# Optimization experiments

Measured on AMD Instinct MI355X. Metric: run time of the kernel, lower is better.

The kernel has to match this reference:

```python
import jax, jax.numpy as jnp
import numpy as np

B, H, W, C = 16, 224, 224, 3
NP = 14                      # n_patches per side
PH = PW = H // NP            # 16
PATCH = PH * PW * C          # 768
D_MODEL = 512
EXPAND = 2
D_INNER = D_MODEL * EXPAND   # 1024
D_STATE = 16
D_CONV = 4
DT_RANK = -(-D_MODEL // 16)  # ceil(512/16) = 32
N_LAYERS = 4
N_CLASSES = 1000


def posemb_sincos_2d(h, w, dim, temperature=10000.0):
    y, x = jnp.meshgrid(jnp.arange(h, dtype=jnp.float32), jnp.arange(w, dtype=jnp.float32), indexing='ij')
    omega = jnp.arange(dim // 4, dtype=jnp.float32) / (dim // 4 - 1)
    omega = 1.0 / (temperature ** omega)
    yy = y.reshape(-1, 1) * omega[None, :]
    xx = x.reshape(-1, 1) * omega[None, :]
    return jnp.concatenate([jnp.sin(xx), jnp.cos(xx), jnp.sin(yy), jnp.cos(yy)], axis=1)  # [h*w, dim]


def setup_inputs() -> dict:
    key = jax.random.key(0)
    ks = jax.random.split(key, 12)
    s = 0.02
    inp = {
        'x': jax.random.normal(ks[0], (B, H, W, C), jnp.float32),
        'patch_w': jax.random.normal(ks[1], (PATCH, D_MODEL), jnp.float32) * s,
        'patch_b': jnp.zeros((D_MODEL,), jnp.float32),
        'norm_w': jnp.ones((N_LAYERS, D_MODEL), jnp.float32),
        'in_proj_w': jax.random.normal(ks[2], (N_LAYERS, D_MODEL, 2 * D_INNER), jnp.float32) * s,
        'conv_w': jax.random.normal(ks[3], (N_LAYERS, D_INNER, D_CONV), jnp.float32) * 0.1,
        'x_proj_w': jax.random.normal(ks[4], (N_LAYERS, D_INNER, DT_RANK + 2 * D_STATE), jnp.float32) * s,
        'dt_proj_w': jax.random.normal(ks[5], (N_LAYERS, DT_RANK, D_INNER), jnp.float32) * s,
        'dt_proj_b': jax.random.normal(ks[6], (N_LAYERS, D_INNER), jnp.float32) * 0.1,
        'A_log': jnp.broadcast_to(jnp.log(jnp.arange(1, D_STATE + 1, dtype=jnp.float32)), (N_LAYERS, D_INNER, D_STATE)) + 0.0,
        'D': jnp.ones((N_LAYERS, D_INNER), jnp.float32),
        'out_proj_w': jax.random.normal(ks[7], (N_LAYERS, D_INNER, D_MODEL), jnp.float32) * s,
        'head_w': jax.random.normal(ks[8], (D_MODEL, N_CLASSES), jnp.float32) * s,
        'head_b': jnp.zeros((N_CLASSES,), jnp.float32),
    }
    return inp


def rms_norm(x, w, eps=1e-5):
    return x * jax.lax.rsqrt(jnp.mean(x * x, axis=-1, keepdims=True) + eps) * w


def selective_scan(u, delta, A, Bm, Cm, Dv):
    # u, delta: [b,l,d]; A: [d,n]; Bm, Cm: [b,l,n]; Dv: [d]
    dA = jnp.exp(jnp.einsum('bld,dn->bldn', delta, A))          # [b,l,d,n]
    dBu = jnp.einsum('bld,bln->bldn', delta * u, Bm)            # [b,l,d,n]
    b, l, d = u.shape
    n = A.shape[1]

    def step(s, inp):
        dA_t, dBu_t, C_t = inp
        s = dA_t * s + dBu_t                                    # [b,d,n]
        y = jnp.einsum('bdn,bn->bd', s, C_t)
        return s, y

    s0 = jnp.zeros((b, d, n), u.dtype)
    _, ys = jax.lax.scan(step, s0, (dA.transpose(1, 0, 2, 3), dBu.transpose(1, 0, 2, 3), Cm.transpose(1, 0, 2)))
    y = ys.transpose(1, 0, 2)                                   # [b,l,d]
    return y + u * Dv


def mamba_block(x, in_w, conv_w, xp_w, dt_w, dt_b, A_log, Dv, out_w):
    b, l, _ = x.shape
    xr = x @ in_w                                               # [b,l,2*d_inner]
    xi, res = jnp.split(xr, 2, axis=-1)
    # causal depthwise conv over sequence
    xc = jax.lax.conv_general_dilated(
        xi.transpose(0, 2, 1),                                  # [b,d_inner,l]
        conv_w[:, None, :],                                     # [d_inner,1,k]
        window_strides=(1,), padding=[(D_CONV - 1, 0)],
        feature_group_count=D_INNER,
        dimension_numbers=('NCH', 'OIH', 'NCH'))
    xi = jax.nn.silu(xc.transpose(0, 2, 1))                     # [b,l,d_inner]
    A = -jnp.exp(A_log)
    x_dbl = xi @ xp_w                                           # [b,l,dt_rank+2n]
    delta, Bm, Cm = jnp.split(x_dbl, [DT_RANK, DT_RANK + D_STATE], axis=-1)
    delta = jax.nn.softplus(delta @ dt_w + dt_b)                # [b,l,d_inner]
    y = selective_scan(xi, delta, A, Bm, Cm, Dv)
    y = y * jax.nn.silu(res)
    return y @ out_w


def reference(x, patch_w, patch_b, norm_w, in_proj_w, conv_w, x_proj_w, dt_proj_w, dt_proj_b, A_log, D, out_proj_w, head_w, head_b):
    b = x.shape[0]
    # patchify: b (h ph) (w pw) c -> b (h w) (ph pw c)
    p = x.reshape(b, NP, PH, NP, PW, C).transpose(0, 1, 3, 2, 4, 5).reshape(b, NP * NP, PATCH)
    h = p @ patch_w + patch_b                                   # [b, 196, d_model]
    h = h + posemb_sincos_2d(NP, NP, D_MODEL)[None]
    for i in range(N_LAYERS):
        h = h + mamba_block(rms_norm(h, norm_w[i]), in_proj_w[i], conv_w[i], x_proj_w[i],
                            dt_proj_w[i], dt_proj_b[i], A_log[i], D[i], out_proj_w[i])
    h = h.mean(axis=1)                                          # [b, d_model]
    return h @ head_w + head_b                                  # [b, n_classes]
```

## Files before the change

kernel.cpp:

```cpp
#include <hip/hip_runtime.h>
#include <hip/hip_bf16.h>
#include <math.h>

#define BATCH 16
#define L_SEQ 196
#define PATCH_DIM 768
#define D_MODEL 512
#define D_INNER 1024
#define D_STATE 16
#define D_CONV 4
#define DT_RANK 32
#define N_LAYERS 4
#define N_CLASSES 1000
#define ROWS (BATCH * L_SEQ)
#define ROWSP 3200
#define NBIG 1152

typedef __hip_bfloat16 bf16;
typedef __attribute__((ext_vector_type(8))) __bf16 bf16x8;
typedef __attribute__((ext_vector_type(8))) short short8;
typedef __attribute__((ext_vector_type(4))) float f32x4;

__device__ __forceinline__ void gload_lds16(const void* g, void* l) {
    __builtin_amdgcn_global_load_lds((const __attribute__((address_space(1))) void*)g,
                                     (__attribute__((address_space(3))) void*)l, 16, 0, 0);
}
__device__ __forceinline__ float bfbits2f(int b) {
    return __int_as_float(((unsigned)b & 0xFFFFu) << 16);
}
__device__ __forceinline__ unsigned short f2bfbits(float f) {
    __hip_bfloat16 h = __float2bfloat16(f);
    return *reinterpret_cast<unsigned short*>(&h);
}

__global__ void patchify_kernel(const float* __restrict__ x, bf16* __restrict__ p) {
    int idx = blockIdx.x * 256 + threadIdx.x;
    if (idx >= ROWS * PATCH_DIM) return;
    int k = idx % PATCH_DIM, row = idx / PATCH_DIM;
    int b = row / L_SEQ, l = row % L_SEQ;
    int i = l / 14, j = l % 14;
    int ph = k / 48, r = k % 48, pw = r / 3, c = r % 3;
    size_t src = (((size_t)b * 224 + i * 16 + ph) * 224 + (j * 16 + pw)) * 3 + c;
    p[idx] = __float2bfloat16(x[src]);
}

__global__ void smallprep_kernel(float* __restrict__ pos,
                                 const float* __restrict__ xpw_all,
                                 bf16* __restrict__ WtBig_all,
                                 const float* __restrict__ cw,
                                 float* __restrict__ cwT) {
    int bid = blockIdx.x, tid = threadIdx.x;
    if (bid < 392) {
        int idx = bid * 256 + tid;
        if (idx >= L_SEQ * D_MODEL) return;
        int l = idx >> 9, col = idx & 511;
        int qd = col >> 7, wi = col & 127;
        float omega = powf(10000.f, -(float)wi / 127.f);
        float yv = (float)(l / 14), xv = (float)(l % 14);
        float arg = (qd < 2 ? xv : yv) * omega;
        pos[idx] = (qd & 1) ? cosf(arg) : sinf(arg);
    } else if (bid < 904) {
        int z = (bid - 392) >> 7;
        int idx = ((bid - 392) & 127) * 256 + tid;
        const float* xpw = xpw_all + (size_t)z * D_INNER * 64;
        bf16* WtBig = WtBig_all + (size_t)z * NBIG * D_INNER;
        int j = idx >> 10, k = idx & 1023;
        int src = (j & 1) ? 48 + (j >> 1) : 32 + (j >> 1);
        WtBig[(size_t)(1024 + j) * 1024 + k] = __float2bfloat16(xpw[k * 64 + src]);
    } else {
        int z = (bid - 904) >> 4;
        int idx = ((bid - 904) & 15) * 256 + tid;
        int d = idx >> 2, k = idx & 3;
        cwT[(size_t)z * 4096 + k * 1024 + d] = cw[(size_t)z * 4096 + d * 4 + k];
    }
}

__global__ __launch_bounds__(256) void transpose_bf16_kernel(
    const float* __restrict__ src, bf16* __restrict__ dst,
    int K, int N, int Npad, size_t src_lstride, size_t dst_lstride)
{
    src += (size_t)blockIdx.z * src_lstride;
    dst += (size_t)blockIdx.z * dst_lstride;
    __shared__ float tile[32][33];
    int kb = blockIdx.y * 32, nb = blockIdx.x * 32;
    int tx = threadIdx.x & 31, ty = threadIdx.x >> 5;
    #pragma unroll
    for (int i = 0; i < 4; ++i) {
        int k = kb + ty + 8 * i, n = nb + tx;
        tile[ty + 8 * i][tx] = (k < K && n < N) ? src[(size_t)k * N + n] : 0.f;
    }
    __syncthreads();
    #pragma unroll
    for (int i = 0; i < 4; ++i) {
        int n = nb + ty + 8 * i, k = kb + tx;
        if (n < Npad && k < K) dst[(size_t)n * K + k] = __float2bfloat16(tile[tx][ty + 8 * i]);
    }
}

__global__ __launch_bounds__(256) void wcomb_kernel(
    const float* __restrict__ xpw_all,
    const float* __restrict__ dtw_all,
    bf16* __restrict__ WtBig_all)
{
    int z = blockIdx.z;
    const float* xpw = xpw_all + (size_t)z * D_INNER * 64;
    const float* dtw = dtw_all + (size_t)z * DT_RANK * D_INNER;
    bf16* Wt = WtBig_all + (size_t)z * NBIG * D_INNER;
    __shared__ float sd[32][17];
    __shared__ float sx[16][33];
    int n0 = blockIdx.x * 16, k0 = blockIdx.y * 16;
    int tid = threadIdx.x;
    {
        int e = tid;        sd[e >> 4][e & 15] = dtw[(e >> 4) * D_INNER + n0 + (e & 15)];
        e = tid + 256;      sd[e >> 4][e & 15] = dtw[(e >> 4) * D_INNER + n0 + (e & 15)];
    }
    {
        int e = tid;        sx[e >> 5][e & 31] = xpw[(size_t)(k0 + (e >> 5)) * 64 + (e & 31)];
        e = tid + 256;      sx[e >> 5][e & 31] = xpw[(size_t)(k0 + (e >> 5)) * 64 + (e & 31)];
    }
    __syncthreads();
    int nn = tid >> 4, kk = tid & 15;
    float acc = 0.f;
    #pragma unroll
    for (int r = 0; r < 32; ++r) acc += sd[r][nn] * sx[kk][r];
    Wt[(size_t)(n0 + nn) * D_INNER + k0 + kk] = __float2bfloat16(acc);
}

template<int MODE, int BM>
__global__ __launch_bounds__(256) void gemm64(
    const bf16* __restrict__ A, const bf16* __restrict__ Wt,
    int K, int gx, int Nstore, int M, int ldc,
    float* __restrict__ Cf, bf16* __restrict__ Cb,
    const float* __restrict__ bias, const float* __restrict__ pos,
    float* __restrict__ Cf2)
{
    constexpr int MI = BM / 32;
    constexpr int NL = (BM == 64) ? 6 : 5;
    int nwg = gridDim.x, bid = blockIdx.x;
    int q = nwg >> 3, r = nwg & 7;
    int xcd = bid & 7, sub = bid >> 3;
    int wgid = (xcd < r ? xcd * (q + 1) : r * (q + 1) + (xcd - r) * q) + sub;
    int bx = wgid % gx, by = wgid / gx;
    int bm = by * BM, bn = bx * 128;

    __shared__ short Als[3][BM * 64];
    __shared__ short Bls[3][128 * 64];
    int tid = threadIdx.x;
    int lane = tid & 63, wid = tid >> 6;
    int wm = wid >> 1, wn = wid & 1;

    int t3 = tid >> 3, t7 = tid & 7;
    int rA0 = t3,      kA0 = t7 ^ (rA0 & 7);
    int rA1 = 32 + t3, kA1 = t7 ^ (rA1 & 7);
    const bf16* gA0 = A + (size_t)(bm + rA0) * K + kA0 * 8;
    const bf16* gA1 = A + (size_t)(bm + rA1) * K + kA1 * 8;
    const int aB0 = (wid * 64) * 8, aB1 = (256 + wid * 64) * 8;
    int rB0 = t3,      kB0 = t7 ^ (rB0 & 7);
    int rB1 = 32 + t3, kB1 = t7 ^ (rB1 & 7);
    int rB2 = 64 + t3, kB2 = t7 ^ (rB2 & 7);
    int rB3 = 96 + t3, kB3 = t7 ^ (rB3 & 7);
    const bf16* gB0 = Wt + (size_t)(bn + rB0) * K + kB0 * 8;
    const bf16* gB1 = Wt + (size_t)(bn + rB1) * K + kB1 * 8;
    const bf16* gB2 = Wt + (size_t)(bn + rB2) * K + kB2 * 8;
    const bf16* gB3 = Wt + (size_t)(bn + rB3) * K + kB3 * 8;
    const int bB0 = (wid * 64) * 8,       bB1 = (256 + wid * 64) * 8;
    const int bB2 = (512 + wid * 64) * 8, bB3 = (768 + wid * 64) * 8;

    auto stage = [&](int buf, int k0) {
        gload_lds16(gA0 + k0, &Als[buf][aB0]);
        if (BM == 64) gload_lds16(gA1 + k0, &Als[buf][aB1]);
        gload_lds16(gB0 + k0, &Bls[buf][bB0]);
        gload_lds16(gB1 + k0, &Bls[buf][bB1]);
        gload_lds16(gB2 + k0, &Bls[buf][bB2]);
        gload_lds16(gB3 + k0, &Bls[buf][bB3]);
    };

    f32x4 acc[MI][4];
    #pragma unroll
    for (int i = 0; i < MI; ++i)
        #pragma unroll
        for (int j = 0; j < 4; ++j)
            acc[i][j] = (f32x4){0.f, 0.f, 0.f, 0.f};

    int nsteps = K >> 6;
    stage(0, 0);
    if (nsteps > 1) stage(1, 64);

    for (int s = 0; s < nsteps; ++s) {
        int buf = s % 3;
        if (s + 2 < nsteps) {
            stage((s + 2) % 3, (s + 2) * 64);
            __builtin_amdgcn_sched_barrier(0);
            asm volatile("s_waitcnt vmcnt(%0)" :: "n"(2 * NL) : "memory");
        } else if (s + 1 < nsteps) {
            asm volatile("s_waitcnt vmcnt(%0)" :: "n"(NL) : "memory");
        } else {
            asm volatile("s_waitcnt vmcnt(0)" ::: "memory");
        }
        __builtin_amdgcn_s_barrier();
        __builtin_amdgcn_sched_barrier(0);

        bf16x8 af[2][MI], bfr[2][4];
        #pragma unroll
        for (int kw = 0; kw < 2; ++kw) {
            int kc = kw * 4 + (lane >> 4);
            #pragma unroll
            for (int mi = 0; mi < MI; ++mi) {
                int row = wm * (BM / 2) + mi * 16 + (lane & 15);
                int kbp = kc ^ (row & 7);
                af[kw][mi] = *reinterpret_cast<const bf16x8*>(&Als[buf][row * 64 + kbp * 8]);
            }
            #pragma unroll
            for (int nj = 0; nj < 4; ++nj) {
                int row = wn * 64 + nj * 16 + (lane & 15);
                int kbp = kc ^ (row & 7);
                bfr[kw][nj] = *reinterpret_cast<const bf16x8*>(&Bls[buf][row * 64 + kbp * 8]);
            }
        }
        #pragma unroll
        for (int kw = 0; kw < 2; ++kw)
            #pragma unroll
            for (int mi = 0; mi < MI; ++mi)
                #pragma unroll
                for (int nj = 0; nj < 4; ++nj)
                    acc[mi][nj] = __builtin_amdgcn_mfma_f32_16x16x32_bf16(af[kw][mi], bfr[kw][nj], acc[mi][nj], 0, 0, 0);

        __builtin_amdgcn_sched_barrier(0);
        __builtin_amdgcn_s_barrier();
    }

    #pragma unroll
    for (int mi = 0; mi < MI; ++mi) {
        #pragma unroll
        for (int nj = 0; nj < 4; ++nj) {
            int r0 = bm + wm * (BM / 2) + mi * 16 + ((lane >> 4) << 2);
            int col = bn + wn * 64 + nj * 16 + (lane & 15);
            if (col >= Nstore) continue;
            #pragma unroll
            for (int j = 0; j < 4; ++j) {
                int row = r0 + j;
                if (row >= M) continue;
                float v = acc[mi][nj][j];
                if (MODE == 4) {
                    if (col < 1024) {
                        float z = v + bias[col];
                        Cf[(size_t)row * 1024 + col] = (z > 20.f) ? z : log1pf(__expf(z));
                    } else {
                        Cf2[(size_t)row * 32 + (col - 1024)] = v;
                    }
                } else {
                    size_t o = (size_t)row * ldc + col;
                    if (MODE == 0) Cb[o] = __float2bfloat16(v);
                    else if (MODE == 2) Cf[o] = v + bias[col] + pos[(size_t)(row % L_SEQ) * D_MODEL + col];
                    else if (MODE == 3) Cf[o] += v;
                }
            }
        }
    }
}

__global__ __launch_bounds__(256) void rmsnorm_kernel(
    const float* __restrict__ h, const float* __restrict__ w, bf16* __restrict__ o)
{
    int row = blockIdx.x;
    int tid = threadIdx.x;
    const float* hr = h + (size_t)row * D_MODEL;
    float v0 = hr[tid], v1 = hr[tid + 256];
    float ss = v0 * v0 + v1 * v1;
    #pragma unroll
    for (int off = 32; off; off >>= 1) ss += __shfl_down(ss, off);
    __shared__ float ls[4];
    __shared__ float scale_s;
    if ((tid & 63) == 0) ls[tid >> 6] = ss;
    __syncthreads();
    if (tid == 0) {
        float t = ls[0] + ls[1] + ls[2] + ls[3];
        scale_s = rsqrtf(t * (1.f / D_MODEL) + 1e-5f);
    }
    __syncthreads();
    float sc = scale_s;
    o[(size_t)row * D_MODEL + tid]       = __float2bfloat16(v0 * sc * w[tid]);
    o[(size_t)row * D_MODEL + tid + 256] = __float2bfloat16(v1 * sc * w[tid + 256]);
}

__global__ __launch_bounds__(256) void conv_silu_kernel(
    const bf16* __restrict__ xr, const float* __restrict__ cwT,
    bf16* __restrict__ xs, unsigned int* __restrict__ ug)
{
    int idx = blockIdx.x * 256 + threadIdx.x;
    if (idx >= ROWS * 128) return;
    int dg = idx & 127, row = idx >> 7;
    int d0 = dg << 3;
    int l = row % L_SEQ;
    float acc[8] = {0.f,0.f,0.f,0.f,0.f,0.f,0.f,0.f};
    #pragma unroll
    for (int k = 0; k < 4; ++k) {
        int ls = l - 3 + k;
        if (ls < 0) continue;
        short8 xv = *reinterpret_cast<const short8*>(xr + (size_t)(row - 3 + k) * 2048 + d0);
        const float* wk = cwT + k * 1024 + d0;
        #pragma unroll
        for (int j = 0; j < 8; ++j)
            acc[j] += bfbits2f(xv[j]) * wk[j];
    }
    short8 rv = *reinterpret_cast<const short8*>(xr + (size_t)row * 2048 + 1024 + d0);
    short8 xsv;
    unsigned ugv[8];
    #pragma unroll
    for (int j = 0; j < 8; ++j) {
        float u = acc[j] / (1.f + __expf(-acc[j]));
        unsigned short ub = f2bfbits(u);
        xsv[j] = (short)ub;
        float res = bfbits2f(rv[j]);
        float g = res / (1.f + __expf(-res));
        ugv[j] = (unsigned)ub | ((unsigned)f2bfbits(g) << 16);
    }
    *reinterpret_cast<short8*>(xs + (size_t)row * 1024 + d0) = xsv;
    uint4* up = reinterpret_cast<uint4*>(ug + (size_t)row * 1024 + d0);
    up[0] = make_uint4(ugv[0], ugv[1], ugv[2], ugv[3]);
    up[1] = make_uint4(ugv[4], ugv[5], ugv[6], ugv[7]);
}

__global__ __launch_bounds__(256) void scan_sp_kernel(
    const unsigned int* __restrict__ ug,
    const float* __restrict__ delta,
    const float* __restrict__ bc,
    const float* __restrict__ A_log,
    const float* __restrict__ Dv,
    bf16* __restrict__ y)
{
    int tid = threadIdx.x;
    int n2 = tid & 7, ch = tid >> 3;
    int b = blockIdx.x >> 5;
    int d = (((int)blockIdx.x & 31) << 5) | ch;
    size_t bbase = (size_t)b * L_SEQ;

    const float L2E = 1.4426950408889634f;
    float A0 = -__expf(A_log[d * 16 + 2 * n2]) * L2E;
    float A1 = -__expf(A_log[d * 16 + 2 * n2 + 1]) * L2E;
    float Dd = Dv[d];
    float s0 = 0.f, s1 = 0.f;

    const unsigned* pu = ug + bbase * 1024 + d;
    const float*    pd = delta + bbase * 1024 + d;
    const float*    pb = bc + bbase * 32 + 4 * n2;
    bf16*           py = y + bbase * 1024 + d;

    unsigned uv[8];
    float dlv[8];
    f32x4 bcv[8];

#define LOADSLOT(i) { \
    uv[i]  = pu[(i) * 1024]; \
    dlv[i] = pd[(i) * 1024]; \
    bcv[i] = *reinterpret_cast<const f32x4*>(pb + (i) * 32); }

#define STEP(i) { \
    float _dl = dlv[i]; \
    float _u  = __int_as_float(uv[i] << 16); \
    float _a0 = __builtin_amdgcn_exp2f(_dl * A0); \
    float _a1 = __builtin_amdgcn_exp2f(_dl * A1); \
    float _du = _dl * _u; \
    s0 = _a0 * s0 + _du * bcv[i].x; \
    s1 = _a1 * s1 + _du * bcv[i].z; \
    float _p = s0 * bcv[i].y + s1 * bcv[i].w; \
    _p += __int_as_float(__builtin_amdgcn_mov_dpp(__float_as_int(_p), 0xB1, 0xF, 0xF, true)); \
    _p += __int_as_float(__builtin_amdgcn_mov_dpp(__float_as_int(_p), 0x4E, 0xF, 0xF, true)); \
    _p += __int_as_float(__builtin_amdgcn_mov_dpp(__float_as_int(_p), 0x141, 0xF, 0xF, true)); \
    if (n2 == 0) { \
        float _g = __int_as_float(uv[i] & 0xFFFF0000u); \
        py[(i) * 1024] = __float2bfloat16((_p + _u * Dd) * _g); \
    } }

    LOADSLOT(0) LOADSLOT(1) LOADSLOT(2) LOADSLOT(3)
    LOADSLOT(4) LOADSLOT(5) LOADSLOT(6) LOADSLOT(7)
    pu += 8 * 1024; pd += 8 * 1024; pb += 8 * 32;

    for (int g = 0; g < 23; ++g) {
        STEP(0) LOADSLOT(0)
        STEP(1) LOADSLOT(1)
        STEP(2) LOADSLOT(2)
        STEP(3) LOADSLOT(3)
        STEP(4) LOADSLOT(4)
        STEP(5) LOADSLOT(5)
        STEP(6) LOADSLOT(6)
        STEP(7) LOADSLOT(7)
        pu += 8 * 1024; pd += 8 * 1024; pb += 8 * 32; py += 8 * 1024;
    }
    STEP(0) LOADSLOT(0)
    STEP(1) LOADSLOT(1)
    STEP(2) LOADSLOT(2)
    STEP(3) LOADSLOT(3)
    STEP(4) STEP(5) STEP(6) STEP(7)
    py += 8 * 1024;
    STEP(0) STEP(1) STEP(2) STEP(3)
#undef LOADSLOT
#undef STEP
}

__global__ __launch_bounds__(256) void mean_kernel(const float* __restrict__ h,
                                                   float* __restrict__ hm) {
    int c = blockIdx.x * 256 + threadIdx.x;
    int b = blockIdx.y;
    const float* hb = h + (size_t)b * L_SEQ * D_MODEL + c;
    float acc = 0.f;
    #pragma unroll 4
    for (int l = 0; l < L_SEQ; ++l) acc += hb[(size_t)l * D_MODEL];
    hm[b * D_MODEL + c] = acc * (1.f / L_SEQ);
}

__global__ __launch_bounds__(256) void head_kernel(
    const float* __restrict__ hm, const float* __restrict__ head_w,
    const float* __restrict__ head_b, float* __restrict__ out)
{
    __shared__ float hmr[D_MODEL];
    int tid = threadIdx.x;
    int b = blockIdx.y;
    hmr[tid]       = hm[b * D_MODEL + tid];
    hmr[tid + 256] = hm[b * D_MODEL + tid + 256];
    __syncthreads();
    int c = blockIdx.x * 256 + tid;
    if (c >= N_CLASSES) return;
    float acc = head_b[c];
    #pragma unroll 8
    for (int k = 0; k < D_MODEL; ++k)
        acc += hmr[k] * head_w[(size_t)k * N_CLASSES + c];
    out[(size_t)b * N_CLASSES + c] = acc;
}

extern "C" void kernel_launch(void* const* d_in, const int* in_sizes, int n_in,
                              void* d_out, int out_size, void* d_ws, size_t ws_size,
                              hipStream_t stream) {
    const float* x         = (const float*)d_in[0];
    const float* patch_w   = (const float*)d_in[1];
    const float* patch_b   = (const float*)d_in[2];
    const float* norm_w    = (const float*)d_in[3];
    const float* in_proj_w = (const float*)d_in[4];
    const float* conv_w    = (const float*)d_in[5];
    const float* x_proj_w  = (const float*)d_in[6];
    const float* dt_proj_w = (const float*)d_in[7];
    const float* dt_proj_b = (const float*)d_in[8];
    const float* A_log     = (const float*)d_in[9];
    const float* Dv        = (const float*)d_in[10];
    const float* out_proj_w= (const float*)d_in[11];
    const float* head_w    = (const float*)d_in[12];
    const float* head_b    = (const float*)d_in[13];
    float* out = (float*)d_out;

    char* base = (char*)d_ws;
    size_t off = 0;
    auto alloc = [&](size_t bytes) -> void* {
        void* p = base + off;
        off += (bytes + 255) & ~(size_t)255;
        return p;
    };
    float* pos   = (float*)alloc((size_t)L_SEQ * D_MODEL * 4);
    bf16*  pwT   = (bf16*) alloc((size_t)D_MODEL * PATCH_DIM * 2);
    bf16*  inT   = (bf16*) alloc((size_t)N_LAYERS * 2 * D_INNER * D_MODEL * 2);
    bf16*  WtBig = (bf16*) alloc((size_t)N_LAYERS * NBIG * D_INNER * 2);
    bf16*  opT   = (bf16*) alloc((size_t)N_LAYERS * D_MODEL * D_INNER * 2);
    float* cwT   = (float*)alloc((size_t)N_LAYERS * 4 * D_INNER * 4);
    float* h     = (float*)alloc((size_t)ROWS * D_MODEL * 4);
    bf16*  xn    = (bf16*) alloc((size_t)ROWSP * D_MODEL * 2);
    char*  reg0  = (char*) alloc((size_t)ROWSP * 2 * D_INNER * 2);
    bf16*  p     = (bf16*)reg0;
    bf16*  xr    = (bf16*)reg0;
    bf16*  xs    = (bf16*) alloc((size_t)ROWSP * D_INNER * 2);
    unsigned int* ug = (unsigned int*)alloc((size_t)ROWSP * D_INNER * 4);
    float* delta = (float*)alloc((size_t)ROWSP * D_INNER * 4);
    float* bcb   = (float*)alloc((size_t)ROWS * 32 * 4);
    bf16*  yb    = (bf16*) alloc((size_t)ROWSP * D_INNER * 2);
    float* hm    = (float*)alloc((size_t)BATCH * D_MODEL * 4);

    patchify_kernel<<<(ROWS * PATCH_DIM + 255) / 256, 256, 0, stream>>>(x, p);
    smallprep_kernel<<<968, 256, 0, stream>>>(pos, x_proj_w, WtBig, conv_w, cwT);
    transpose_bf16_kernel<<<dim3(16, 24), 256, 0, stream>>>(
        patch_w, pwT, PATCH_DIM, D_MODEL, D_MODEL, 0, 0);
    transpose_bf16_kernel<<<dim3(64, 16, N_LAYERS), 256, 0, stream>>>(
        in_proj_w, inT, D_MODEL, 2 * D_INNER, 2 * D_INNER,
        (size_t)D_MODEL * 2 * D_INNER, (size_t)2 * D_INNER * D_MODEL);
    transpose_bf16_kernel<<<dim3(16, 32, N_LAYERS), 256, 0, stream>>>(
        out_proj_w, opT, D_INNER, D_MODEL, D_MODEL,
        (size_t)D_INNER * D_MODEL, (size_t)D_MODEL * D_INNER);
    wcomb_kernel<<<dim3(64, 64, N_LAYERS), 256, 0, stream>>>(
        x_proj_w, dt_proj_w, WtBig);

    gemm64<2, 32><<<(D_MODEL / 128) * (ROWSP / 32), 256, 0, stream>>>(
        p, pwT, PATCH_DIM, D_MODEL / 128, D_MODEL, ROWS, D_MODEL,
        h, nullptr, patch_b, pos, nullptr);

    for (int layer = 0; layer < N_LAYERS; ++layer) {
        rmsnorm_kernel<<<ROWS, 256, 0, stream>>>(h, norm_w + layer * D_MODEL, xn);

        gemm64<0, 64><<<(2 * D_INNER / 128) * (ROWSP / 64), 256, 0, stream>>>(
            xn, inT + (size_t)layer * 2 * D_INNER * D_MODEL,
            D_MODEL, 2 * D_INNER / 128, 2 * D_INNER, ROWS, 2 * D_INNER,
            nullptr, xr, nullptr, nullptr, nullptr);

        conv_silu_kernel<<<(ROWS * 128 + 255) / 256, 256, 0, stream>>>(
            xr, cwT + (size_t)layer * 4 * D_INNER, xs, ug);

        gemm64<4, 64><<<(NBIG / 128) * (ROWSP / 64), 256, 0, stream>>>(
            xs, WtBig + (size_t)layer * NBIG * D_INNER,
            D_INNER, NBIG / 128, 1056, ROWS, 0,
            delta, nullptr, dt_proj_b + (size_t)layer * D_INNER, nullptr, bcb);

        scan_sp_kernel<<<BATCH * (D_INNER / 32), 256, 0, stream>>>(
            ug, delta, bcb,
            A_log + (size_t)layer * D_INNER * D_STATE,
            Dv + (size_t)layer * D_INNER, yb);

        gemm64<3, 32><<<(D_MODEL / 128) * (ROWSP / 32), 256, 0, stream>>>(
            yb, opT + (size_t)layer * D_MODEL * D_INNER,
            D_INNER, D_MODEL / 128, D_MODEL, ROWS, D_MODEL,
            h, nullptr, nullptr, nullptr, nullptr);
    }

    mean_kernel<<<dim3(2, BATCH), 256, 0, stream>>>(h, hm);
    head_kernel<<<dim3(4, BATCH), 256, 0, stream>>>(hm, head_w, head_b, out);
}
```

Before: 546.0 us.

## Retile wcomb, use one wavefront per row in rmsnorm, widen scan state per thread

Three separate kernels change. The wcomb weight-combination kernel now computes a 32x32 tile with a 2x2 register block per thread instead of one output per thread. The rmsnorm kernel now handles one row per wavefront using vectorized loads and stores and a shuffle-only reduction, which removes the shared-memory barriers. The selective scan now gives each thread 4 state elements instead of 2, with 4 threads per channel and 64 channels per block. This halves the lane count and cuts one DPP reduction step, at the cost of more registers and fewer blocks.

After: 523.9 us. 1.04x faster.

```diff
diff --git a/kernel.cpp b/kernel.cpp
--- a/kernel.cpp
+++ b/kernel.cpp
@@ -106,24 +106,31 @@
     const float* xpw = xpw_all + (size_t)z * D_INNER * 64;
     const float* dtw = dtw_all + (size_t)z * DT_RANK * D_INNER;
     bf16* Wt = WtBig_all + (size_t)z * NBIG * D_INNER;
-    __shared__ float sd[32][17];
-    __shared__ float sx[16][33];
-    int n0 = blockIdx.x * 16, k0 = blockIdx.y * 16;
+    __shared__ float sd[32][33];
+    __shared__ float sx[32][33];
+    int n0 = blockIdx.x * 32, k0 = blockIdx.y * 32;
     int tid = threadIdx.x;
-    {
-        int e = tid;        sd[e >> 4][e & 15] = dtw[(e >> 4) * D_INNER + n0 + (e & 15)];
-        e = tid + 256;      sd[e >> 4][e & 15] = dtw[(e >> 4) * D_INNER + n0 + (e & 15)];
-    }
-    {
-        int e = tid;        sx[e >> 5][e & 31] = xpw[(size_t)(k0 + (e >> 5)) * 64 + (e & 31)];
-        e = tid + 256;      sx[e >> 5][e & 31] = xpw[(size_t)(k0 + (e >> 5)) * 64 + (e & 31)];
+    #pragma unroll
+    for (int i = 0; i < 4; ++i) {
+        int e = tid + 256 * i;
+        sd[e >> 5][e & 31] = dtw[(size_t)(e >> 5) * D_INNER + n0 + (e & 31)];
+        sx[e >> 5][e & 31] = xpw[(size_t)(k0 + (e >> 5)) * 64 + (e & 31)];
     }
     __syncthreads();
-    int nn = tid >> 4, kk = tid & 15;
-    float acc = 0.f;
-    #pragma unroll
-    for (int r = 0; r < 32; ++r) acc += sd[r][nn] * sx[kk][r];
-    Wt[(size_t)(n0 + nn) * D_INNER + k0 + kk] = __float2bfloat16(acc);
+    int ty = tid >> 4, tx = tid & 15;
+    int nn = ty * 2, kk = tx * 2;
+    float a00 = 0.f, a01 = 0.f, a10 = 0.f, a11 = 0.f;
+    #pragma unroll
+    for (int r = 0; r < 32; ++r) {
+        float d0 = sd[r][nn], d1 = sd[r][nn + 1];
+        float x0 = sx[kk][r], x1 = sx[kk + 1][r];
+        a00 += d0 * x0; a01 += d0 * x1;
+        a10 += d1 * x0; a11 += d1 * x1;
+    }
+    Wt[(size_t)(n0 + nn) * D_INNER + k0 + kk]           = __float2bfloat16(a00);
+    Wt[(size_t)(n0 + nn) * D_INNER + k0 + kk + 1]       = __float2bfloat16(a01);
+    Wt[(size_t)(n0 + nn + 1) * D_INNER + k0 + kk]       = __float2bfloat16(a10);
+    Wt[(size_t)(n0 + nn + 1) * D_INNER + k0 + kk + 1]   = __float2bfloat16(a11);
 }
 
 template<int MODE, int BM>
@@ -262,25 +269,29 @@
 __global__ __launch_bounds__(256) void rmsnorm_kernel(
     const float* __restrict__ h, const float* __restrict__ w, bf16* __restrict__ o)
 {
-    int row = blockIdx.x;
-    int tid = threadIdx.x;
-    const float* hr = h + (size_t)row * D_MODEL;
-    float v0 = hr[tid], v1 = hr[tid + 256];
-    float ss = v0 * v0 + v1 * v1;
-    #pragma unroll
-    for (int off = 32; off; off >>= 1) ss += __shfl_down(ss, off);
-    __shared__ float ls[4];
-    __shared__ float scale_s;
-    if ((tid & 63) == 0) ls[tid >> 6] = ss;
-    __syncthreads();
-    if (tid == 0) {
-        float t = ls[0] + ls[1] + ls[2] + ls[3];
-        scale_s = rsqrtf(t * (1.f / D_MODEL) + 1e-5f);
-    }
-    __syncthreads();
-    float sc = scale_s;
-    o[(size_t)row * D_MODEL + tid]       = __float2bfloat16(v0 * sc * w[tid]);
-    o[(size_t)row * D_MODEL + tid + 256] = __float2bfloat16(v1 * sc * w[tid + 256]);
+    int row = (blockIdx.x << 2) | (threadIdx.x >> 6);
+    int lane = threadIdx.x & 63;
+    const float* hr = h + (size_t)row * D_MODEL + lane * 8;
+    f32x4 v0 = *reinterpret_cast<const f32x4*>(hr);
+    f32x4 v1 = *reinterpret_cast<const f32x4*>(hr + 4);
+    float ss = v0.x*v0.x + v0.y*v0.y + v0.z*v0.z + v0.w*v0.w
+             + v1.x*v1.x + v1.y*v1.y + v1.z*v1.z + v1.w*v1.w;
+    #pragma unroll
+    for (int off = 32; off; off >>= 1) ss += __shfl_xor(ss, off);
+    float sc = rsqrtf(ss * (1.f / D_MODEL) + 1e-5f);
+    const float* wr = w + lane * 8;
+    f32x4 w0 = *reinterpret_cast<const f32x4*>(wr);
+    f32x4 w1 = *reinterpret_cast<const f32x4*>(wr + 4);
+    short8 ov;
+    ov[0] = (short)f2bfbits(v0.x * sc * w0.x);
+    ov[1] = (short)f2bfbits(v0.y * sc * w0.y);
+    ov[2] = (short)f2bfbits(v0.z * sc * w0.z);
+    ov[3] = (short)f2bfbits(v0.w * sc * w0.w);
+    ov[4] = (short)f2bfbits(v1.x * sc * w1.x);
+    ov[5] = (short)f2bfbits(v1.y * sc * w1.y);
+    ov[6] = (short)f2bfbits(v1.z * sc * w1.z);
+    ov[7] = (short)f2bfbits(v1.w * sc * w1.w);
+    *reinterpret_cast<short8*>(o + (size_t)row * D_MODEL + lane * 8) = ov;
 }
 
 __global__ __launch_bounds__(256) void conv_silu_kernel(
@@ -330,44 +341,52 @@
     bf16* __restrict__ y)
 {
     int tid = threadIdx.x;
-    int n2 = tid & 7, ch = tid >> 3;
-    int b = blockIdx.x >> 5;
-    int d = (((int)blockIdx.x & 31) << 5) | ch;
+    int n3 = tid & 3, ch = tid >> 2;
+    int b = blockIdx.x >> 4;
+    int d = (((int)blockIdx.x & 15) << 6) | ch;
     size_t bbase = (size_t)b * L_SEQ;
 
     const float L2E = 1.4426950408889634f;
-    float A0 = -__expf(A_log[d * 16 + 2 * n2]) * L2E;
-    float A1 = -__expf(A_log[d * 16 + 2 * n2 + 1]) * L2E;
+    float A0 = -__expf(A_log[d * 16 + 4 * n3])     * L2E;
+    float A1 = -__expf(A_log[d * 16 + 4 * n3 + 1]) * L2E;
+    float A2 = -__expf(A_log[d * 16 + 4 * n3 + 2]) * L2E;
+    float A3 = -__expf(A_log[d * 16 + 4 * n3 + 3]) * L2E;
     float Dd = Dv[d];
-    float s0 = 0.f, s1 = 0.f;
+    float s0 = 0.f, s1 = 0.f, s2 = 0.f, s3 = 0.f;
 
     const unsigned* pu = ug + bbase * 1024 + d;
     const float*    pd = delta + bbase * 1024 + d;
-    const float*    pb = bc + bbase * 32 + 4 * n2;
+    const float*    pb = bc + bbase * 32 + 8 * n3;
     bf16*           py = y + bbase * 1024 + d;
 
     unsigned uv[8];
     float dlv[8];
-    f32x4 bcv[8];
+    f32x4 bc0[8], bc1[8];
 
 #define LOADSLOT(i) { \
     uv[i]  = pu[(i) * 1024]; \
     dlv[i] = pd[(i) * 1024]; \
-    bcv[i] = *reinterpret_cast<const f32x4*>(pb + (i) * 32); }
+    bc0[i] = *reinterpret_cast<const f32x4*>(pb + (i) * 32); \
+    bc1[i] = *reinterpret_cast<const f32x4*>(pb + (i) * 32 + 4); }
 
 #define STEP(i) { \
     float _dl = dlv[i]; \
     float _u  = __int_as_float(uv[i] << 16); \
     float _a0 = __builtin_amdgcn_exp2f(_dl * A0); \
     float _a1 = __builtin_amdgcn_exp2f(_dl * A1); \
+    float _a2 = __builtin_amdgcn_exp2f(_dl * A2); \
+    float _a3 = __builtin_amdgcn_exp2f(_dl * A3); \
     float _du = _dl * _u; \
-    s0 = _a0 * s0 + _du * bcv[i].x; \
-    s1 = _a1 * s1 + _du * bcv[i].z; \
-    float _p = s0 * bcv[i].y + s1 * bcv[i].w; \
+    s0 = _a0 * s0 + _du * bc0[i].x; \
+    s1 = _a1 * s1 + _du * bc0[i].z; \
+    s2 = _a2 * s2 + _du * bc1[i].x; \
+    s3 = _a3 * s3 + _du * bc1[i].z; \
+    float _p  = s0 * bc0[i].y + s1 * bc0[i].w; \
+    float _p2 = s2 * bc1[i].y + s3 * bc1[i].w; \
+    _p += _p2; \
     _p += __int_as_float(__builtin_amdgcn_mov_dpp(__float_as_int(_p), 0xB1, 0xF, 0xF, true)); \
     _p += __int_as_float(__builtin_amdgcn_mov_dpp(__float_as_int(_p), 0x4E, 0xF, 0xF, true)); \
-    _p += __int_as_float(__builtin_amdgcn_mov_dpp(__float_as_int(_p), 0x141, 0xF, 0xF, true)); \
-    if (n2 == 0) { \
+    if (n3 == 0) { \
         float _g = __int_as_float(uv[i] & 0xFFFF0000u); \
         py[(i) * 1024] = __float2bfloat16((_p + _u * Dd) * _g); \
     } }
@@ -482,7 +501,7 @@
     transpose_bf16_kernel<<<dim3(16, 32, N_LAYERS), 256, 0, stream>>>(
         out_proj_w, opT, D_INNER, D_MODEL, D_MODEL,
         (size_t)D_INNER * D_MODEL, (size_t)D_MODEL * D_INNER);
-    wcomb_kernel<<<dim3(64, 64, N_LAYERS), 256, 0, stream>>>(
+    wcomb_kernel<<<dim3(32, 32, N_LAYERS), 256, 0, stream>>>(
         x_proj_w, dt_proj_w, WtBig);
 
     gemm64<2, 32><<<(D_MODEL / 128) * (ROWSP / 32), 256, 0, stream>>>(
@@ -490,7 +509,7 @@
         h, nullptr, patch_b, pos, nullptr);
 
     for (int layer = 0; layer < N_LAYERS; ++layer) {
-        rmsnorm_kernel<<<ROWS, 256, 0, stream>>>(h, norm_w + layer * D_MODEL, xn);
+        rmsnorm_kernel<<<ROWS / 4, 256, 0, stream>>>(h, norm_w + layer * D_MODEL, xn);
 
         gemm64<0, 64><<<(2 * D_INNER / 128) * (ROWSP / 64), 256, 0, stream>>>(
             xn, inT + (size_t)layer * 2 * D_INNER * D_MODEL,
@@ -505,7 +524,7 @@
             D_INNER, NBIG / 128, 1056, ROWS, 0,
             delta, nullptr, dt_proj_b + (size_t)layer * D_INNER, nullptr, bcb);
 
-        scan_sp_kernel<<<BATCH * (D_INNER / 32), 256, 0, stream>>>(
+        scan_sp_kernel<<<BATCH * (D_INNER / 64), 256, 0, stream>>>(
             ug, delta, bcb,
             A_log + (size_t)layer * D_INNER * D_STATE,
             Dv + (size_t)layer * D_INNER, yb);
```
